# Performance work log

Measured on AMD Instinct MI355X. Metric: run time of the kernel, lower is better.

Reference implementation:

```python
import jax, jax.numpy as jnp
import numpy as np

N_NODES = 5000
N_EDGES = 50000
HIDDEN = 64
EDGE_DIM = 16


def setup_inputs() -> dict:
    key = jax.random.key(0)
    ks = jax.random.split(key, 8)
    d = HIDDEN
    h = jax.random.normal(ks[0], (N_NODES, d), dtype=jnp.float32)
    edge_index = jax.random.randint(ks[1], (2, N_EDGES), 0, N_NODES, dtype=jnp.int64)
    edge_features = jax.random.normal(ks[2], (N_EDGES, EDGE_DIM), dtype=jnp.float32)
    # edge-network MLP: Linear(edge_dim, d) -> ReLU -> Linear(d, d*d)
    W1 = jax.random.normal(ks[3], (EDGE_DIM, d), dtype=jnp.float32) * (1.0 / np.sqrt(EDGE_DIM))
    b1 = jnp.zeros((d,), dtype=jnp.float32)
    W2 = jax.random.normal(ks[4], (d, d * d), dtype=jnp.float32) * (1.0 / np.sqrt(d))
    b2 = jnp.zeros((d * d,), dtype=jnp.float32)
    # GRUCell params (torch layout: rows = [reset; update; new])
    W_ih = jax.random.normal(ks[5], (3 * d, d), dtype=jnp.float32) * (1.0 / np.sqrt(d))
    W_hh = jax.random.normal(ks[6], (3 * d, d), dtype=jnp.float32) * (1.0 / np.sqrt(d))
    b_ih = jnp.zeros((3 * d,), dtype=jnp.float32)
    b_hh = jnp.zeros((3 * d,), dtype=jnp.float32)
    return {"h": h, "edge_index": edge_index, "edge_features": edge_features,
            "W1": W1, "b1": b1, "W2": W2, "b2": b2,
            "W_ih": W_ih, "W_hh": W_hh, "b_ih": b_ih, "b_hh": b_hh}


def reference(h, edge_index, edge_features, W1, b1, W2, b2, W_ih, W_hh, b_ih, b_hh):
    n_nodes, d = h.shape
    src, tgt = edge_index[0], edge_index[1]
    # 1) gather sender states
    h_w = h[src]  # (E, d)
    # 2-3) edge MLP -> per-edge transformation matrices (E, d, d)
    A = jax.nn.relu(edge_features @ W1 + b1) @ W2 + b2
    A = A.reshape(-1, d, d)
    # 4) per-edge matvec messages
    msg = jnp.einsum('eij,ej->ei', A, h_w)  # (E, d)
    # 5) scatter-sum aggregation per target node
    m = jax.ops.segment_sum(msg, tgt, num_segments=n_nodes)  # (N, d)
    # 6) GRUCell(m, h) - torch semantics
    gi = m @ W_ih.T + b_ih   # (N, 3d)
    gh = h @ W_hh.T + b_hh   # (N, 3d)
    i_r, i_z, i_n = jnp.split(gi, 3, axis=-1)
    h_r, h_z, h_n = jnp.split(gh, 3, axis=-1)
    r = jax.nn.sigmoid(i_r + h_r)
    z = jax.nn.sigmoid(i_z + h_z)
    n = jnp.tanh(i_n + r * h_n)
    h_new = (1.0 - z) * n + z * h
    return h_new
```

## Files before the change

### kernel.cpp

```cpp
#include <hip/hip_runtime.h>
#include <math.h>

#define N_NODES 5000
#define N_EDGES 50000
#define EB 192
#define POISON_I ((int)0xAAAAAAAAu)

typedef _Float16 f16x8 __attribute__((ext_vector_type(8)));
typedef _Float16 f16x2 __attribute__((ext_vector_type(2)));
typedef float    f32x4 __attribute__((ext_vector_type(4)));

static __device__ __forceinline__ f32x4 mfma16f(f16x8 a, f16x8 b, f32x4 c) {
    return __builtin_amdgcn_mfma_f32_16x16x32_f16(a, b, c, 0, 0, 0);
}

__global__ void prep_kernel(const float* __restrict__ W2, const float* __restrict__ b2,
                            const float* __restrict__ Wih, const float* __restrict__ Whh,
                            const int* __restrict__ ei,
                            _Float16* __restrict__ Br, _Float16* __restrict__ Bg2,
                            int* __restrict__ cnt) {
    int g = blockIdx.x * 256 + threadIdx.x;
    if (g < 33792) {
        int nt = g / 8448, rem = g - nt * 8448;
        int ks = rem >> 6, lane = rem & 63;
        int lo = lane & 15, q = lane >> 4;
        int i = nt * 16 + lo, kap0 = ks * 32 + q * 8;
        f16x8 v;
#pragma unroll
        for (int p = 0; p < 8; ++p) {
            int kap = kap0 + p;
            int k2 = kap >> 7, rem2 = kap & 127;
            int j = rem2 >> 1, k = k2 * 2 + (rem2 & 1);
            float x = 0.f;
            if (k < 64) x = W2[(size_t)k * 4096 + i * 64 + j];
            else if (k == 64) x = b2[i * 64 + j];
            v[p] = (_Float16)x;
        }
        *(f16x8*)(Br + (size_t)g * 8) = v;
        return;
    }
    g -= 33792;
    if (g < 3072) {
        int ct = g >> 7, ks = (g >> 6) & 1, lane = g & 63;
        int lo = lane & 15, q = lane >> 4;
        const float* src = (ct < 12) ? Wih : Whh;
        int r = ((ct < 12) ? ct : ct - 12) * 16 + lo;
        int j0 = ks * 32 + q * 8;
        f16x8 v;
#pragma unroll
        for (int p = 0; p < 8; ++p) v[p] = (_Float16)src[r * 64 + j0 + p];
        *(f16x8*)(Bg2 + (size_t)g * 8) = v;
        return;
    }
    g -= 3072;
    if (g < N_EDGES) atomicAdd(&cnt[ei[N_EDGES + g]], 1);
}

__global__ __launch_bounds__(1024) void scan_kernel(const int* __restrict__ cnt,
                                                    int* __restrict__ off,
                                                    int* __restrict__ cur) {
    __shared__ int s[1024];
    int tid = threadIdx.x;
    int base = tid * 5;
    int loc[5]; int sum = 0;
#pragma unroll
    for (int q = 0; q < 5; ++q) {
        int v = (base + q < N_NODES) ? (cnt[base + q] - POISON_I) : 0;
        loc[q] = sum; sum += v;
    }
    s[tid] = sum; __syncthreads();
    for (int d = 1; d < 1024; d <<= 1) {
        int v = (tid >= d) ? s[tid - d] : 0;
        __syncthreads();
        s[tid] += v;
        __syncthreads();
    }
    int excl = (tid > 0) ? s[tid - 1] : 0;
#pragma unroll
    for (int q = 0; q < 5; ++q)
        if (base + q < N_NODES) { off[base + q] = excl + loc[q]; cur[base + q] = excl + loc[q]; }
    if (tid == 1023) off[N_NODES] = excl + sum;
}

__global__ void scatter_kernel(const int* __restrict__ ei, int* __restrict__ cur,
                               int* __restrict__ srcp, int* __restrict__ eidp) {
    int e = blockIdx.x * 256 + threadIdx.x;
    if (e < N_EDGES) {
        int q = atomicAdd(&cur[ei[N_EDGES + e]], 1);
        srcp[q] = ei[e];
        eidp[q] = e;
    }
}

__global__ __launch_bounds__(1024, 4) void fused_gnn(
    const int* __restrict__ toff, const int* __restrict__ srcp,
    const int* __restrict__ eidp, const float* __restrict__ ef,
    const float* __restrict__ W1, const float* __restrict__ b1,
    const float* __restrict__ h, const _Float16* __restrict__ Br,
    const _Float16* __restrict__ Bg2, const float* __restrict__ bih,
    const float* __restrict__ bhh, float* __restrict__ out)
{
    extern __shared__ __align__(16) char smem[];
    _Float16* As    = (_Float16*)smem;
    float*    tfs   = (float*)(smem + 33024);
    float*    hfsT  = (float*)(smem + 82176);
    int*      sidxb = (int*)smem;
    int*      eidxb = sidxb + 4096;
    float*    mbuf  = (float*)(smem + 33024);
    _Float16* mls   = (_Float16*)(smem + 33024 + 12480);
    _Float16* hls16 = (_Float16*)(smem + 33024 + 14784);
    float*    gbuf  = (float*)(smem + 33024 + 17088);

    int tid = threadIdx.x, w16 = tid >> 6, lane = tid & 63;
    int lo = lane & 15, q = lane >> 4;
    int nt = w16 & 3, kq = w16 >> 2;
    int m0 = blockIdx.x * 16;

    int E0 = toff[m0];
    int mhi = m0 + 16; if (mhi > N_NODES) mhi = N_NODES;
    int etot = toff[mhi] - E0;
    int na = m0 + w16;     if (na > N_NODES) na = N_NODES;
    int nb = na + 1;       if (nb > N_NODES) nb = N_NODES;
    int ns0 = toff[na] - E0, ns1 = toff[nb] - E0;

    for (int i2 = tid; i2 < etot; i2 += 1024) {
        sidxb[i2] = srcp[E0 + i2];
        eidxb[i2] = eidp[E0 + i2];
    }

    float w1c[16];
#pragma unroll
    for (int k = 0; k < 16; ++k) w1c[k] = W1[k * 64 + lane];
    float b1l = b1[lane];

    float gacc[64];
#pragma unroll
    for (int k = 0; k < 64; ++k) gacc[k] = 0.f;
    float sacc = 0.f;
    __syncthreads();

    int nbat = (etot + EB - 1) / EB;
    for (int b = 0; b < nbat; ++b) {
        int ebase = b * EB;
        int bcnt = etot - ebase; if (bcnt > EB) bcnt = EB;
        if (b) __syncthreads();
        for (int r = 0; r < EB / 16; ++r) {
            int eloc = r * 16 + w16;
            if (eloc < bcnt) {
                int src = sidxb[ebase + eloc];
                int eid = eidxb[ebase + eloc];
                hfsT[lane * 193 + eloc] = h[(size_t)src * 64 + lane];
                const float* efr = ef + (size_t)eid * 16;
                f32x4 e0v = *(const f32x4*)(efr);
                f32x4 e1v = *(const f32x4*)(efr + 4);
                f32x4 e2v = *(const f32x4*)(efr + 8);
                f32x4 e3v = *(const f32x4*)(efr + 12);
                float tacc = b1l;
#pragma unroll
                for (int k = 0; k < 4; ++k) {
                    tacc += e0v[k] * w1c[k] + e1v[k] * w1c[4 + k]
                          + e2v[k] * w1c[8 + k] + e3v[k] * w1c[12 + k];
                }
                tfs[eloc * 64 + lane] = fmaxf(tacc, 0.f);
            }
        }
        __syncthreads();
        int e0 = ns0 - ebase; if (e0 < 0) e0 = 0;
        int e1 = ns1 - ebase; if (e1 > bcnt) e1 = bcnt;
        for (int e = e0; e < e1; ++e) {
            float hj = hfsT[lane * 193 + e];
            const f32x4* tr = (const f32x4*)&tfs[e * 64];
#pragma unroll
            for (int v4 = 0; v4 < 16; ++v4) {
                f32x4 tv = tr[v4];
#pragma unroll
                for (int kk = 0; kk < 4; ++kk)
                    gacc[v4 * 4 + kk] += tv[kk] * hj;
            }
            sacc += hj;
        }
    }
    __syncthreads();

    const f16x8* BrV = (const f16x8*)Br;
    f32x4 macc = {0.f, 0.f, 0.f, 0.f};
#pragma unroll
    for (int kc = 0; kc < 4; ++kc) {
        _Float16* aw = As + w16 * 1032;
#pragma unroll
        for (int k2l = 0; k2l < 8; ++k2l) {
            int k = (kc * 8 + k2l) * 2;
            f16x2 pv = { (_Float16)gacc[k], (_Float16)gacc[k + 1] };
            *(f16x2*)(aw + k2l * 128 + lane * 2) = pv;
        }
        __syncthreads();
        const _Float16* Arow = As + lo * 1032 + q * 8;
#pragma unroll
        for (int s = 0; s < 8; ++s) {
            int ksl = kq * 8 + s;
            f16x8 a = *(const f16x8*)(Arow + ksl * 32);
            f16x8 bfr = BrV[(size_t)(nt * 132 + kc * 32 + ksl) * 64 + lane];
            macc = mfma16f(a, bfr, macc);
        }
        __syncthreads();
    }
    {
        f16x2 pv = { (_Float16)sacc, (_Float16)0.f };
        *(f16x2*)(As + w16 * 1032 + lane * 2) = pv;
    }
    __syncthreads();
    {
        f16x8 a = *(const f16x8*)(As + lo * 1032 + kq * 32 + q * 8);
        f16x8 bfr = BrV[(size_t)(nt * 132 + 128 + kq) * 64 + lane];
        macc = mfma16f(a, bfr, macc);
    }
    __syncthreads();
    if (kq > 0) {
#pragma unroll
        for (int g = 0; g < 4; ++g)
            mbuf[(kq - 1) * 1040 + (q * 4 + g) * 65 + nt * 16 + lo] = macc[g];
    }
    if (kq == 3) {
        int t2 = nt * 64 + lane;
#pragma unroll
        for (int r = 0; r < 4; ++r) {
            int e2 = r * 256 + t2, nl = e2 >> 6, j = e2 & 63;
            int n = m0 + nl;
            float hv = (n < N_NODES) ? h[(size_t)n * 64 + j] : 0.f;
            hls16[nl * 72 + j] = (_Float16)hv;
        }
    }
    __syncthreads();
    if (kq == 0) {
#pragma unroll
        for (int g = 0; g < 4; ++g) {
            float mv = macc[g];
#pragma unroll
            for (int pp = 0; pp < 3; ++pp)
                mv += mbuf[pp * 1040 + (q * 4 + g) * 65 + nt * 16 + lo];
            mls[(q * 4 + g) * 72 + nt * 16 + lo] = (_Float16)mv;
        }
    }
    __syncthreads();
    if (w16 < 8) {
        int w8 = w16;
        f16x8 am0 = *(const f16x8*)&mls[lo * 72 + q * 8];
        f16x8 am1 = *(const f16x8*)&mls[lo * 72 + 32 + q * 8];
        f16x8 ah0 = *(const f16x8*)&hls16[lo * 72 + q * 8];
        f16x8 ah1 = *(const f16x8*)&hls16[lo * 72 + 32 + q * 8];
        const f16x8* BgV = (const f16x8*)Bg2;
        f32x4 z4 = {0.f, 0.f, 0.f, 0.f};
        f32x4 ga[3] = {z4, z4, z4};
#pragma unroll
        for (int j = 0; j < 3; ++j) {
            int ct = w8 + 8 * j;
            f16x8 bg0 = BgV[(size_t)(ct * 2 + 0) * 64 + lane];
            f16x8 bg1 = BgV[(size_t)(ct * 2 + 1) * 64 + lane];
            f16x8 a0f = (ct < 12) ? am0 : ah0;
            f16x8 a1f = (ct < 12) ? am1 : ah1;
            ga[j] = mfma16f(a0f, bg0, ga[j]);
            ga[j] = mfma16f(a1f, bg1, ga[j]);
        }
#pragma unroll
        for (int j = 0; j < 3; ++j) {
            int ct = w8 + 8 * j;
            int col = (ct < 12) ? (ct * 16 + lo) : (192 + (ct - 12) * 16 + lo);
#pragma unroll
            for (int g = 0; g < 4; ++g) gbuf[(q * 4 + g) * 385 + col] = ga[j][g];
        }
    }
    __syncthreads();
    if (w16 < 8) {
        int i = lane;
#pragma unroll
        for (int u = 0; u < 2; ++u) {
            int nl = w16 * 2 + u, n = m0 + nl;
            if (n >= N_NODES) continue;
            const float* gb = gbuf + nl * 385;
            float ir  = gb[i]       + bih[i];
            float iz  = gb[64 + i]  + bih[64 + i];
            float inn = gb[128 + i] + bih[128 + i];
            float hr  = gb[192 + i] + bhh[i];
            float hz  = gb[256 + i] + bhh[64 + i];
            float hn  = gb[320 + i] + bhh[128 + i];
            float hval = h[(size_t)n * 64 + i];
            float r = 1.f / (1.f + expf(-(ir + hr)));
            float z = 1.f / (1.f + expf(-(iz + hz)));
            float nn = tanhf(inn + r * hn);
            out[n * 64 + i] = (1.f - z) * nn + z * hval;
        }
    }
}

extern "C" void kernel_launch(void* const* d_in, const int* in_sizes, int n_in,
                              void* d_out, int out_size, void* d_ws, size_t ws_size,
                              hipStream_t stream) {
    const float* h   = (const float*)d_in[0];
    const int*   ei  = (const int*)d_in[1];
    const float* ef  = (const float*)d_in[2];
    const float* W1  = (const float*)d_in[3];
    const float* b1  = (const float*)d_in[4];
    const float* W2  = (const float*)d_in[5];
    const float* b2  = (const float*)d_in[6];
    const float* Wih = (const float*)d_in[7];
    const float* Whh = (const float*)d_in[8];
    const float* bih = (const float*)d_in[9];
    const float* bhh = (const float*)d_in[10];
    float* out = (float*)d_out;

    _Float16* Br   = (_Float16*)d_ws;
    _Float16* Bg2  = Br + 270336;
    int*      cnt  = (int*)(Bg2 + 24576);
    int*      toff = cnt + N_NODES;
    int*      cur  = toff + N_NODES + 1;
    int*      srcp = cur + N_NODES;
    int*      eidp = srcp + N_EDGES;

    static bool lds_cfg = false;
    if (!lds_cfg) {
        hipFuncSetAttribute((const void*)fused_gnn,
                            hipFuncAttributeMaxDynamicSharedMemorySize, 131584);
        lds_cfg = true;
    }

    prep_kernel<<<340, 256, 0, stream>>>(W2, b2, Wih, Whh, ei, Br, Bg2, cnt);
    scan_kernel<<<1, 1024, 0, stream>>>(cnt, toff, cur);
    scatter_kernel<<<196, 256, 0, stream>>>(ei, cur, srcp, eidp);
    fused_gnn<<<313, 1024, 131584, stream>>>(toff, srcp, eidp, ef, W1, b1, h,
                                             Br, Bg2, bih, bhh, out);
}
```

Measured before the change: 144.5 us.

## Compute per-node edge outer-product accumulation with MFMA using split-f16 h

Replaces the per-wave scalar FMA loop, which builds each node's 64x64 accumulator of t⊗h over its incoming edges, with 16x16x16 f16 MFMA tiles. Edges are laid out in padded per-node windows of 16 slots in LDS. h is split into high and low f16 parts to keep accuracy close to fp32, and t is rounded to f16. This also removes the shared index staging and shrinks LDS use. In exchange it does twice the MFMA work for the split, pays for padding when nodes have uneven degree, and adds f16 rounding error on t.

```diff
diff --git a/kernel.cpp b/kernel.cpp
--- a/kernel.cpp
+++ b/kernel.cpp
@@ -3,15 +3,18 @@
 
 #define N_NODES 5000
 #define N_EDGES 50000
-#define EB 192
 #define POISON_I ((int)0xAAAAAAAAu)
 
 typedef _Float16 f16x8 __attribute__((ext_vector_type(8)));
+typedef _Float16 f16x4 __attribute__((ext_vector_type(4)));
 typedef _Float16 f16x2 __attribute__((ext_vector_type(2)));
 typedef float    f32x4 __attribute__((ext_vector_type(4)));
 
 static __device__ __forceinline__ f32x4 mfma16f(f16x8 a, f16x8 b, f32x4 c) {
     return __builtin_amdgcn_mfma_f32_16x16x32_f16(a, b, c, 0, 0, 0);
+}
+static __device__ __forceinline__ f32x4 mfma16k16(f16x4 a, f16x4 b, f32x4 c) {
+    return __builtin_amdgcn_mfma_f32_16x16x16f16(a, b, c, 0, 0, 0);
 }
 
 __global__ void prep_kernel(const float* __restrict__ W2, const float* __restrict__ b2,
@@ -101,11 +104,11 @@
     const float* __restrict__ bhh, float* __restrict__ out)
 {
     extern __shared__ __align__(16) char smem[];
-    _Float16* As    = (_Float16*)smem;
-    float*    tfs   = (float*)(smem + 33024);
-    float*    hfsT  = (float*)(smem + 82176);
-    int*      sidxb = (int*)smem;
-    int*      eidxb = sidxb + 4096;
+    _Float16* tS  = (_Float16*)(smem);
+    _Float16* hHi = (_Float16*)(smem + 33280);
+    _Float16* hLo = (_Float16*)(smem + 66560);
+    int*      nsl = (int*)(smem + 99840);
+    _Float16* As    = (_Float16*)(smem);
     float*    mbuf  = (float*)(smem + 33024);
     _Float16* mls   = (_Float16*)(smem + 33024 + 12480);
     _Float16* hls16 = (_Float16*)(smem + 33024 + 14784);
@@ -116,68 +119,83 @@
     int nt = w16 & 3, kq = w16 >> 2;
     int m0 = blockIdx.x * 16;
 
-    int E0 = toff[m0];
-    int mhi = m0 + 16; if (mhi > N_NODES) mhi = N_NODES;
-    int etot = toff[mhi] - E0;
-    int na = m0 + w16;     if (na > N_NODES) na = N_NODES;
-    int nb = na + 1;       if (nb > N_NODES) nb = N_NODES;
-    int ns0 = toff[na] - E0, ns1 = toff[nb] - E0;
-
-    for (int i2 = tid; i2 < etot; i2 += 1024) {
-        sidxb[i2] = srcp[E0 + i2];
-        eidxb[i2] = eidp[E0 + i2];
-    }
-
+    if (tid < 17) {
+        int nn = m0 + tid; if (nn > N_NODES) nn = N_NODES;
+        nsl[tid] = toff[nn];
+    }
     float w1c[16];
 #pragma unroll
     for (int k = 0; k < 16; ++k) w1c[k] = W1[k * 64 + lane];
     float b1l = b1[lane];
 
-    float gacc[64];
-#pragma unroll
-    for (int k = 0; k < 64; ++k) gacc[k] = 0.f;
+    f32x4 z4 = {0.f, 0.f, 0.f, 0.f};
+    f32x4 acc[4][4];
+#pragma unroll
+    for (int a = 0; a < 4; ++a)
+#pragma unroll
+        for (int b = 0; b < 4; ++b) acc[a][b] = z4;
     float sacc = 0.f;
     __syncthreads();
 
-    int nbat = (etot + EB - 1) / EB;
-    for (int b = 0; b < nbat; ++b) {
-        int ebase = b * EB;
-        int bcnt = etot - ebase; if (bcnt > EB) bcnt = EB;
-        if (b) __syncthreads();
-        for (int r = 0; r < EB / 16; ++r) {
-            int eloc = r * 16 + w16;
-            if (eloc < bcnt) {
-                int src = sidxb[ebase + eloc];
-                int eid = eidxb[ebase + eloc];
-                hfsT[lane * 193 + eloc] = h[(size_t)src * 64 + lane];
+    int nwin = 0;
+    {
+        int mx = 0;
+#pragma unroll
+        for (int n = 0; n < 16; ++n) {
+            int c = nsl[n + 1] - nsl[n];
+            if (c > mx) mx = c;
+        }
+        nwin = (mx + 15) >> 4;
+    }
+
+    for (int ws = 0; ws < nwin; ++ws) {
+        if (ws) __syncthreads();
+        int epos = ws * 16 + w16;
+#pragma unroll 4
+        for (int r = 0; r < 16; ++r) {
+            int base = nsl[r], cnt2 = nsl[r + 1] - base;
+            int cc = r * 16 + w16;
+            if (epos < cnt2) {
+                int ge = __builtin_amdgcn_readfirstlane(base + epos);
+                int src = srcp[ge], eid = eidp[ge];
+                float hv = h[(size_t)src * 64 + lane];
+                _Float16 hh = (_Float16)hv;
+                _Float16 hl = (_Float16)(hv - (float)hh);
                 const float* efr = ef + (size_t)eid * 16;
-                f32x4 e0v = *(const f32x4*)(efr);
-                f32x4 e1v = *(const f32x4*)(efr + 4);
-                f32x4 e2v = *(const f32x4*)(efr + 8);
-                f32x4 e3v = *(const f32x4*)(efr + 12);
                 float tacc = b1l;
 #pragma unroll
-                for (int k = 0; k < 4; ++k) {
-                    tacc += e0v[k] * w1c[k] + e1v[k] * w1c[4 + k]
-                          + e2v[k] * w1c[8 + k] + e3v[k] * w1c[12 + k];
-                }
-                tfs[eloc * 64 + lane] = fmaxf(tacc, 0.f);
+                for (int k = 0; k < 16; ++k) tacc += efr[k] * w1c[k];
+                tS [lane * 260 + cc] = (_Float16)fmaxf(tacc, 0.f);
+                hHi[lane * 260 + cc] = hh;
+                hLo[lane * 260 + cc] = hl;
+            } else {
+                tS [lane * 260 + cc] = (_Float16)0.f;
+                hHi[lane * 260 + cc] = (_Float16)0.f;
+                hLo[lane * 260 + cc] = (_Float16)0.f;
             }
         }
         __syncthreads();
-        int e0 = ns0 - ebase; if (e0 < 0) e0 = 0;
-        int e1 = ns1 - ebase; if (e1 > bcnt) e1 = bcnt;
-        for (int e = e0; e < e1; ++e) {
-            float hj = hfsT[lane * 193 + e];
-            const f32x4* tr = (const f32x4*)&tfs[e * 64];
-#pragma unroll
-            for (int v4 = 0; v4 < 16; ++v4) {
-                f32x4 tv = tr[v4];
-#pragma unroll
-                for (int kk = 0; kk < 4; ++kk)
-                    gacc[v4 * 4 + kk] += tv[kk] * hj;
+        int cb = w16 * 16 + q * 4;
+        f16x4 at[4];
+#pragma unroll
+        for (int mi = 0; mi < 4; ++mi)
+            at[mi] = *(const f16x4*)&tS[(mi * 16 + lo) * 260 + cb];
+#pragma unroll
+        for (int ni = 0; ni < 4; ++ni) {
+            f16x4 bh = *(const f16x4*)&hHi[(ni * 16 + lo) * 260 + cb];
+            f16x4 bl = *(const f16x4*)&hLo[(ni * 16 + lo) * 260 + cb];
+#pragma unroll
+            for (int mi = 0; mi < 4; ++mi) {
+                acc[mi][ni] = mfma16k16(at[mi], bh, acc[mi][ni]);
+                acc[mi][ni] = mfma16k16(at[mi], bl, acc[mi][ni]);
             }
-            sacc += hj;
+        }
+#pragma unroll
+        for (int t4 = 0; t4 < 4; ++t4) {
+            f16x4 a4 = *(const f16x4*)&hHi[lane * 260 + w16 * 16 + t4 * 4];
+            f16x4 b4 = *(const f16x4*)&hLo[lane * 260 + w16 * 16 + t4 * 4];
+#pragma unroll
+            for (int i = 0; i < 4; ++i) sacc += (float)a4[i] + (float)b4[i];
         }
     }
     __syncthreads();
@@ -188,11 +206,13 @@
     for (int kc = 0; kc < 4; ++kc) {
         _Float16* aw = As + w16 * 1032;
 #pragma unroll
-        for (int k2l = 0; k2l < 8; ++k2l) {
-            int k = (kc * 8 + k2l) * 2;
-            f16x2 pv = { (_Float16)gacc[k], (_Float16)gacc[k + 1] };
-            *(f16x2*)(aw + k2l * 128 + lane * 2) = pv;
-        }
+        for (int ni = 0; ni < 4; ++ni)
+#pragma unroll
+            for (int g0 = 0; g0 < 4; g0 += 2) {
+                int k2l = q * 2 + (g0 >> 1);
+                f16x2 pv = { (_Float16)acc[kc][ni][g0], (_Float16)acc[kc][ni][g0 + 1] };
+                *(f16x2*)(aw + k2l * 128 + (ni * 16 + lo) * 2) = pv;
+            }
         __syncthreads();
         const _Float16* Arow = As + lo * 1032 + q * 8;
 #pragma unroll
@@ -249,7 +269,6 @@
         f16x8 ah0 = *(const f16x8*)&hls16[lo * 72 + q * 8];
         f16x8 ah1 = *(const f16x8*)&hls16[lo * 72 + 32 + q * 8];
         const f16x8* BgV = (const f16x8*)Bg2;
-        f32x4 z4 = {0.f, 0.f, 0.f, 0.f};
         f32x4 ga[3] = {z4, z4, z4};
 #pragma unroll
         for (int j = 0; j < 3; ++j) {
@@ -319,13 +338,13 @@
     static bool lds_cfg = false;
     if (!lds_cfg) {
         hipFuncSetAttribute((const void*)fused_gnn,
-                            hipFuncAttributeMaxDynamicSharedMemorySize, 131584);
+                            hipFuncAttributeMaxDynamicSharedMemorySize, 99968);
         lds_cfg = true;
     }
 
     prep_kernel<<<340, 256, 0, stream>>>(W2, b2, Wih, Whh, ei, Br, Bg2, cnt);
     scan_kernel<<<1, 1024, 0, stream>>>(cnt, toff, cur);
     scatter_kernel<<<196, 256, 0, stream>>>(ei, cur, srcp, eidp);
-    fused_gnn<<<313, 1024, 131584, stream>>>(toff, srcp, eidp, ef, W1, b1, h,
-                                             Br, Bg2, bih, bhh, out);
-}
+    fused_gnn<<<313, 1024, 99968, stream>>>(toff, srcp, eidp, ef, W1, b1, h,
+                                            Br, Bg2, bih, bhh, out);
+}
```

Measured after the change: 130.5 us, median of 2. 9.7% less time.
